# Kernel optimization log

Measured on AMD Instinct MI355X. Metric: run time of the kernel, lower is better.

## Reference

```python
import jax, jax.numpy as jnp
import numpy as np

B, S, H = 32, 4096, 512
N = 2 * H  # n = hidden_size * 2


def setup_inputs() -> dict:
    key = jax.random.key(0)
    ks = jax.random.split(key, 10)
    scale = 1.0 / np.sqrt(N)
    return {
        "dec_in_state": jax.random.normal(ks[0], (B, N), jnp.float32),
        "enc_states": jax.random.normal(ks[1], (B, S, N), jnp.float32),
        "enc_lens": jax.random.randint(ks[2], (B,), 1, S + 1),
        "coverage_vector": jax.random.uniform(ks[3], (B, S), jnp.float32),
        "Wh": jax.random.normal(ks[4], (N, N), jnp.float32) * scale,
        "bh": jnp.zeros((N,), jnp.float32),
        "Ws": jax.random.normal(ks[5], (N, N), jnp.float32) * scale,
        "bs": jnp.zeros((N,), jnp.float32),
        "wc": jax.random.normal(ks[6], (N,), jnp.float32) * scale,  # W_c: Linear(1, N, bias=False)
        "v": jax.random.normal(ks[7], (N,), jnp.float32) * scale,   # v: Linear(N, 1, bias=False)
    }


def reference(dec_in_state, enc_states, enc_lens, coverage_vector, Wh, bh, Ws, bs, wc, v):
    seq_len = enc_states.shape[1]
    # additive Bahdanau features: [B,S,N]
    enc_feats = jnp.einsum("bsn,mn->bsm", enc_states, Wh) + bh
    dec_feats = dec_in_state @ Ws.T + bs  # [B,N]
    cov_feats = coverage_vector[..., None] * wc  # [B,S,N] (Linear(1,N,no bias))
    e = jnp.tanh(enc_feats + dec_feats[:, None, :] + cov_feats) @ v  # [B,S]
    # masked renormalized softmax
    mask = (jnp.arange(seq_len)[None, :] < enc_lens[:, None]).astype(e.dtype)  # [B,S]
    attn = jax.nn.softmax(e, axis=1) * mask
    attn = attn / attn.sum(axis=1, keepdims=True)
    context = jnp.einsum("bs,bsn->bn", attn, enc_states)  # [B,N]
    coverage_out = coverage_vector + attn
    return (context, attn, coverage_out)
```

## Files before the change

kernel.cpp:

```cpp
#include <hip/hip_runtime.h>
#include <math.h>

#define B 32
#define S 4096
#define N 1024

typedef short short8 __attribute__((ext_vector_type(8)));
typedef short short4v __attribute__((ext_vector_type(4)));
typedef float float4v __attribute__((ext_vector_type(4)));

__device__ inline short f2bf(float f) {
    unsigned u = __builtin_bit_cast(unsigned, f);
    u += 0x7fffu + ((u >> 16) & 1u);
    return (short)(u >> 16);
}

__device__ __forceinline__ void load_lds16(const void* g, void* l) {
    __builtin_amdgcn_global_load_lds(
        (const __attribute__((address_space(1))) void*)g,
        (__attribute__((address_space(3))) void*)l, 16, 0, 0);
}

__global__ __launch_bounds__(256)
void prep_cvt_kernel(const float* __restrict__ dec, const float* __restrict__ Ws,
                     const float* __restrict__ bs, const float* __restrict__ enc,
                     const float* __restrict__ Wh, float* __restrict__ dec_feats,
                     float* __restrict__ e, short* __restrict__ encb,
                     short* __restrict__ whb) {
    unsigned bid = blockIdx.x;
    int tid = threadIdx.x;
    if (bid < 2048u) {
        if (bid < 512u) e[bid * 256 + tid] = 0.f;
        const size_t n8e = (size_t)B * S * N / 8;
        for (size_t i = (size_t)bid * 256 + tid; i < n8e; i += 2048u * 256u) {
            const float4v* s = (const float4v*)(enc + i * 8);
            float4v a = s[0], b = s[1];
            short8 o = { f2bf(a.x), f2bf(a.y), f2bf(a.z), f2bf(a.w),
                         f2bf(b.x), f2bf(b.y), f2bf(b.z), f2bf(b.w) };
            *(short8*)(encb + i * 8) = o;
        }
    } else if (bid < 2064u) {
        const size_t n8w = (size_t)N * N / 8;
        for (size_t i = (size_t)(bid - 2048u) * 256 + tid; i < n8w; i += 16u * 256u) {
            const float4v* s = (const float4v*)(Wh + i * 8);
            float4v a = s[0], b = s[1];
            short8 o = { f2bf(a.x), f2bf(a.y), f2bf(a.z), f2bf(a.w),
                         f2bf(b.x), f2bf(b.y), f2bf(b.z), f2bf(b.w) };
            *(short8*)(whb + i * 8) = o;
        }
    } else {
        int wid  = (int)(bid - 2064u) * 4 + (tid >> 6);
        int lane = tid & 63;
        int m = wid >> 5, b = wid & 31;
        const float4* drow = (const float4*)(dec + (size_t)b * N);
        const float4* wrow = (const float4*)(Ws + (size_t)m * N);
        float acc = 0.f;
#pragma unroll
        for (int k = 0; k < 4; ++k) {
            float4 a = drow[lane + (k << 6)];
            float4 w = wrow[lane + (k << 6)];
            acc += a.x * w.x + a.y * w.y + a.z * w.z + a.w * w.w;
        }
        acc += __shfl_xor(acc, 1);  acc += __shfl_xor(acc, 2);
        acc += __shfl_xor(acc, 4);  acc += __shfl_xor(acc, 8);
        acc += __shfl_xor(acc, 16); acc += __shfl_xor(acc, 32);
        if (lane == 0) dec_feats[(size_t)b * N + m] = acc + bs[m];
    }
}

__global__ __launch_bounds__(256)
void prep_kernel(const float* __restrict__ dec, const float* __restrict__ Ws,
                 const float* __restrict__ bs, float* __restrict__ dec_feats,
                 float* __restrict__ e) {
    int tg = blockIdx.x * 256 + threadIdx.x;
    if (tg < B * S) e[tg] = 0.f;
    int wid  = (blockIdx.x << 2) + (threadIdx.x >> 6);
    int lane = threadIdx.x & 63;
    int m = wid >> 5, b = wid & 31;
    const float4* drow = (const float4*)(dec + (size_t)b * N);
    const float4* wrow = (const float4*)(Ws + (size_t)m * N);
    float acc = 0.f;
#pragma unroll
    for (int k = 0; k < 4; ++k) {
        float4 a = drow[lane + (k << 6)];
        float4 w = wrow[lane + (k << 6)];
        acc += a.x * w.x + a.y * w.y + a.z * w.z + a.w * w.w;
    }
    acc += __shfl_xor(acc, 1);  acc += __shfl_xor(acc, 2);
    acc += __shfl_xor(acc, 4);  acc += __shfl_xor(acc, 8);
    acc += __shfl_xor(acc, 16); acc += __shfl_xor(acc, 32);
    if (lane == 0) dec_feats[(size_t)b * N + m] = acc + bs[m];
}

#define REGION_A(slot, hk) ((slot)*16384 + (hk)*8192)
#define REGION_B(slot, hk) (32768 + (slot)*16384 + (hk)*8192)

__global__ __launch_bounds__(512, 2)
void score_mfma8_kernel(const short* __restrict__ encb, const short* __restrict__ whb,
                        const float* __restrict__ bh, const float* __restrict__ dec_feats,
                        const float* __restrict__ cov, const float* __restrict__ wc,
                        const float* __restrict__ v, float* __restrict__ e) {
    __shared__ short lds[65536];

    unsigned bid = blockIdx.x;
    unsigned c = (bid & 7u) * 128u + (bid >> 3);
    int rtp = (int)(c >> 2), mtile = (int)(c & 3u);
    int m0 = mtile * 256;

    int t = threadIdx.x, lane = t & 63, w = t >> 6;
    int wm_ = w >> 2, wn_ = w & 3;
    int cq = lane >> 4, cm = lane & 15;

    int srow = lane >> 2;
    int sg = (lane & 3) ^ ((lane >> 3) & 3);
    const short* bS0 = whb + (size_t)(m0 + w * 16 + srow) * N + sg * 8;
    const short* bS1 = bS0 + (size_t)128 * N;
    const int dc0 = w * 512, dc1 = dc0 + 4096;

    int aoff[8], boff[4];
#pragma unroll
    for (int f = 0; f < 8; ++f) {
        int R = wm_ * 128 + f * 16 + cm;
        aoff[f] = R * 32 + ((cq ^ ((R >> 1) & 3)) << 3);
    }
#pragma unroll
    for (int j = 0; j < 4; ++j) {
        int R = wn_ * 64 + j * 16 + cm;
        boff[j] = R * 32 + ((cq ^ ((R >> 1) & 3)) << 3);
    }

    float basej[4], wcj[4], vj[4];
    {
        int bidx0 = (rtp * 2 * 256) >> 12;
        const float* df = dec_feats + ((size_t)bidx0 << 10);
#pragma unroll
        for (int j = 0; j < 4; ++j) {
            int m = m0 + wn_ * 64 + j * 16 + cm;
            basej[j] = bh[m] + df[m];
            wcj[j]   = wc[m];
            vj[j]    = v[m];
        }
    }

#define STAGE(srcp0, srcp1, region, colElem) do {                         \
        int _cc = (colElem) & (N - 1);                                    \
        load_lds16((srcp0) + _cc, &lds[(region) + dc0]);                  \
        load_lds16((srcp1) + _cc, &lds[(region) + dc1]);                  \
    } while (0)

#define PHASE(slot, sub, SRC0, SRC1, SREGION, SCOL) do {                      \
        const int hk_ = (sub) >> 1, mh_ = (sub) & 1;                          \
        if (mh_ == 0) {                                                       \
            _Pragma("unroll")                                                 \
            for (int j = 0; j < 4; ++j)                                       \
                bf[j] = *(const short8*)&lds[REGION_B(slot, hk_) + boff[j]];  \
        }                                                                     \
        short8 af[4];                                                         \
        _Pragma("unroll")                                                     \
        for (int f = 0; f < 4; ++f)                                           \
            af[f] = *(const short8*)&lds[REGION_A(slot, hk_) + aoff[mh_ * 4 + f]]; \
        STAGE(SRC0, SRC1, SREGION, SCOL);                                     \
        __builtin_amdgcn_s_barrier();                                         \
        asm volatile("s_waitcnt lgkmcnt(0)" ::: "memory");                    \
        __builtin_amdgcn_sched_barrier(0);                                    \
        __builtin_amdgcn_s_setprio(1);                                        \
        _Pragma("unroll")                                                     \
        for (int f = 0; f < 4; ++f)                                           \
            _Pragma("unroll")                                                 \
            for (int j = 0; j < 4; ++j)                                       \
                acc[mh_ * 4 + f][j] = __builtin_amdgcn_mfma_f32_16x16x32_bf16(\
                    af[f], bf[j], acc[mh_ * 4 + f][j], 0, 0, 0);              \
        __builtin_amdgcn_s_setprio(0);                                        \
        if (mh_ == 1) asm volatile("s_waitcnt vmcnt(8)" ::: "memory");        \
        __builtin_amdgcn_s_barrier();                                         \
    } while (0)

#pragma unroll 1
    for (int it = 0; it < 2; ++it) {
        int r0 = (rtp * 2 + it) * 256;
        const short* aS0 = encb + (size_t)(r0 + w * 16 + srow) * N + sg * 8;
        const short* aS1 = aS0 + (size_t)128 * N;

        float4v acc[8][4];
#pragma unroll
        for (int f = 0; f < 8; ++f)
#pragma unroll
            for (int j = 0; j < 4; ++j) acc[f][j] = (float4v){0.f, 0.f, 0.f, 0.f};

        STAGE(aS0, aS1, REGION_A(0, 0), 0);
        STAGE(bS0, bS1, REGION_B(0, 0), 0);
        STAGE(aS0, aS1, REGION_A(0, 1), 32);
        STAGE(bS0, bS1, REGION_B(0, 1), 32);
        STAGE(aS0, aS1, REGION_A(1, 0), 64);
        STAGE(bS0, bS1, REGION_B(1, 0), 64);
        asm volatile("s_waitcnt vmcnt(8)" ::: "memory");
        __builtin_amdgcn_s_barrier();

        short8 bf[4];

#pragma unroll 1
        for (int i = 0; i < 8; ++i) {
            int kb = i * 128;
            PHASE(0, 0, aS0, aS1, REGION_A(1, 1), kb + 96);
            PHASE(0, 1, bS0, bS1, REGION_B(1, 1), kb + 96);
            PHASE(0, 2, aS0, aS1, REGION_A(0, 0), kb + 128);
            PHASE(0, 3, bS0, bS1, REGION_B(0, 0), kb + 128);
            PHASE(1, 0, aS0, aS1, REGION_A(0, 1), kb + 160);
            PHASE(1, 1, bS0, bS1, REGION_B(0, 1), kb + 160);
            PHASE(1, 2, aS0, aS1, REGION_A(1, 0), kb + 192);
            PHASE(1, 3, bS0, bS1, REGION_B(1, 0), kb + 192);
        }
        asm volatile("s_waitcnt vmcnt(0)" ::: "memory");

#pragma unroll
        for (int f = 0; f < 8; ++f) {
            int rbase = r0 + wm_ * 128 + f * 16 + cq * 4;
            float4v cvv = *(const float4v*)&cov[rbase];
            float cv[4] = {cvv.x, cvv.y, cvv.z, cvv.w};
            float rs[4] = {0.f, 0.f, 0.f, 0.f};
#pragma unroll
            for (int j = 0; j < 4; ++j) {
#pragma unroll
                for (int reg = 0; reg < 4; ++reg) {
                    float val = acc[f][j][reg] + basej[j] + cv[reg] * wcj[j];
                    val = fminf(fmaxf(val, -15.f), 15.f);
                    float t2 = __builtin_amdgcn_exp2f(val * 2.8853900817779268f);
                    float r  = __builtin_amdgcn_rcpf(t2 + 1.f);
                    float th = fmaf(-2.f, r, 1.f);
                    rs[reg] = fmaf(th, vj[j], rs[reg]);
                }
            }
#pragma unroll
            for (int reg = 0; reg < 4; ++reg) {
                float p = rs[reg];
                p += __shfl_xor(p, 1);
                p += __shfl_xor(p, 2);
                p += __shfl_xor(p, 4);
                p += __shfl_xor(p, 8);
                if (cm == 0) atomicAdd(&e[rbase + reg], p);
            }
        }
        asm volatile("s_waitcnt vmcnt(0)" ::: "memory");
        __builtin_amdgcn_s_barrier();
    }
#undef PHASE
#undef STAGE
}

#define BR 128
#define BM 128
#define BK 64
#define LDK (BK + 8)

__global__ __launch_bounds__(256)
void score_mfma_kernel(const float* __restrict__ enc, const float* __restrict__ Wh,
                       const float* __restrict__ bh, const float* __restrict__ dec_feats,
                       const float* __restrict__ cov, const float* __restrict__ wc,
                       const float* __restrict__ v, float* __restrict__ e) {
    __shared__ short As[BR][LDK];
    __shared__ short Bs[BM][LDK];

    unsigned h   = blockIdx.x;
    unsigned xcd = h & 7u;
    unsigned mt  = (h >> 3) & 7u;
    unsigned g   = h >> 6;
    int r0 = (int)(xcd + 8u * g) * BR;
    int m0 = (int)mt * BM;

    int t    = threadIdx.x;
    int lane = t & 63;
    int w    = t >> 6;
    int wr   = (w >> 1) * 64;
    int wm   = (w & 1) * 64;
    int cq   = lane >> 4;
    int cm   = lane & 15;

    float4v acc[4][4];
#pragma unroll
    for (int i = 0; i < 4; ++i)
#pragma unroll
        for (int j = 0; j < 4; ++j) acc[i][j] = (float4v){0.f, 0.f, 0.f, 0.f};

    int srow = t >> 4;
    int scol = (t & 15) * 4;

    for (int k0 = 0; k0 < N; k0 += BK) {
#pragma unroll
        for (int p = 0; p < 8; ++p) {
            int row = p * 16 + srow;
            float4v a = *(const float4v*)(enc + (size_t)(r0 + row) * N + k0 + scol);
            short4v ap = { f2bf(a.x), f2bf(a.y), f2bf(a.z), f2bf(a.w) };
            *(short4v*)&As[row][scol] = ap;
            float4v bq = *(const float4v*)(Wh + (size_t)(m0 + row) * N + k0 + scol);
            short4v bp = { f2bf(bq.x), f2bf(bq.y), f2bf(bq.z), f2bf(bq.w) };
            *(short4v*)&Bs[row][scol] = bp;
        }
        __syncthreads();
#pragma unroll
        for (int ks = 0; ks < BK; ks += 32) {
            short8 af[4], bfr[4];
#pragma unroll
            for (int i = 0; i < 4; ++i)
                af[i] = *(const short8*)&As[wr + i * 16 + cm][ks + cq * 8];
#pragma unroll
            for (int j = 0; j < 4; ++j)
                bfr[j] = *(const short8*)&Bs[wm + j * 16 + cm][ks + cq * 8];
#pragma unroll
            for (int i = 0; i < 4; ++i)
#pragma unroll
                for (int j = 0; j < 4; ++j)
                    acc[i][j] = __builtin_amdgcn_mfma_f32_16x16x32_bf16(
                        af[i], bfr[j], acc[i][j], 0, 0, 0);
        }
        __syncthreads();
    }

    int b = r0 >> 12;
    const float* df = dec_feats + ((size_t)b << 10);

    float basej[4], wcj[4], vj[4];
#pragma unroll
    for (int j = 0; j < 4; ++j) {
        int m = m0 + wm + j * 16 + cm;
        basej[j] = bh[m] + df[m];
        wcj[j]   = wc[m];
        vj[j]    = v[m];
    }

#pragma unroll
    for (int i = 0; i < 4; ++i) {
        int rbase = r0 + wr + i * 16 + cq * 4;
        float cv[4];
#pragma unroll
        for (int reg = 0; reg < 4; ++reg) cv[reg] = cov[rbase + reg];
        float rs[4] = {0.f, 0.f, 0.f, 0.f};
#pragma unroll
        for (int j = 0; j < 4; ++j) {
#pragma unroll
            for (int reg = 0; reg < 4; ++reg) {
                float val = acc[i][j][reg] + basej[j] + cv[reg] * wcj[j];
                val = fminf(fmaxf(val, -15.f), 15.f);
                float t2 = __builtin_amdgcn_exp2f(val * 2.8853900817779268f);
                float r  = __builtin_amdgcn_rcpf(t2 + 1.f);
                float th = fmaf(-2.f, r, 1.f);
                rs[reg] = fmaf(th, vj[j], rs[reg]);
            }
        }
#pragma unroll
        for (int reg = 0; reg < 4; ++reg) {
            float p = rs[reg];
            p += __shfl_xor(p, 1);
            p += __shfl_xor(p, 2);
            p += __shfl_xor(p, 4);
            p += __shfl_xor(p, 8);
            if (cm == 0) atomicAdd(&e[rbase + reg], p);
        }
    }
}

__global__ __launch_bounds__(1024)
void softmax_kernel(const float* __restrict__ e, const int* __restrict__ lens,
                    const float* __restrict__ cov,
                    float* __restrict__ attn, float* __restrict__ cov_out) {
    int b = blockIdx.x, t = threadIdx.x;
    int lane = t & 63, wid = t >> 6;
    int len = lens[b];
    const float* eb = e + (size_t)b * S;
    __shared__ float redm[16], reds[16];

    float ev[4];
    float mx = -INFINITY;
#pragma unroll
    for (int k = 0; k < 4; ++k) {
        int s = t + (k << 10);
        ev[k] = (s < len) ? eb[s] : -INFINITY;
        mx = fmaxf(mx, ev[k]);
    }
    mx = fmaxf(mx, __shfl_xor(mx, 1));  mx = fmaxf(mx, __shfl_xor(mx, 2));
    mx = fmaxf(mx, __shfl_xor(mx, 4));  mx = fmaxf(mx, __shfl_xor(mx, 8));
    mx = fmaxf(mx, __shfl_xor(mx, 16)); mx = fmaxf(mx, __shfl_xor(mx, 32));
    if (lane == 0) redm[wid] = mx;
    __syncthreads();
    if (t < 16) {
        float v2 = redm[t];
        v2 = fmaxf(v2, __shfl_xor(v2, 1)); v2 = fmaxf(v2, __shfl_xor(v2, 2));
        v2 = fmaxf(v2, __shfl_xor(v2, 4)); v2 = fmaxf(v2, __shfl_xor(v2, 8));
        if (t == 0) redm[0] = v2;
    }
    __syncthreads();
    mx = redm[0];

    float ex[4];
    float sum = 0.f;
#pragma unroll
    for (int k = 0; k < 4; ++k) {
        ex[k] = exp2f((ev[k] - mx) * 1.4426950408889634f);
        sum += ex[k];
    }
    sum += __shfl_xor(sum, 1);  sum += __shfl_xor(sum, 2);
    sum += __shfl_xor(sum, 4);  sum += __shfl_xor(sum, 8);
    sum += __shfl_xor(sum, 16); sum += __shfl_xor(sum, 32);
    if (lane == 0) reds[wid] = sum;
    __syncthreads();
    if (t < 16) {
        float v2 = reds[t];
        v2 += __shfl_xor(v2, 1); v2 += __shfl_xor(v2, 2);
        v2 += __shfl_xor(v2, 4); v2 += __shfl_xor(v2, 8);
        if (t == 0) reds[0] = v2;
    }
    __syncthreads();
    float inv = 1.f / reds[0];

#pragma unroll
    for (int k = 0; k < 4; ++k) {
        int s = t + (k << 10);
        float a = ex[k] * inv;
        attn[(size_t)b * S + s] = a;
        cov_out[(size_t)b * S + s] = cov[(size_t)b * S + s] + a;
    }
}

#define SCH 64
__global__ __launch_bounds__(256)
void context_part_kernel(const float* __restrict__ attn, const float* __restrict__ enc,
                         float* __restrict__ part) {
    int b  = blockIdx.y;
    int ch = blockIdx.x;
    int s0 = ch * (S / SCH);
    int n4 = threadIdx.x;
    const float4* ep = (const float4*)(enc + ((size_t)b * S + s0) * N);
    float4 acc = {0.f, 0.f, 0.f, 0.f};
    for (int s = 0; s < S / SCH; ++s) {
        float a = attn[(size_t)b * S + s0 + s];
        float4 ev = ep[(size_t)s * (N / 4) + n4];
        acc.x += a * ev.x; acc.y += a * ev.y;
        acc.z += a * ev.z; acc.w += a * ev.w;
    }
    *(float4*)&part[((size_t)b * SCH + ch) * N + n4 * 4] = acc;
}

__global__ __launch_bounds__(256)
void context_reduce_kernel(const float* __restrict__ part, float* __restrict__ ctx) {
    int idx = blockIdx.x * 256 + threadIdx.x;
    int b = idx >> 10, n = idx & (N - 1);
    const float* p = part + (size_t)b * SCH * N + n;
    float acc = 0.f;
#pragma unroll
    for (int c2 = 0; c2 < SCH; ++c2) acc += p[(size_t)c2 * N];
    ctx[idx] = acc;
}

__global__ __launch_bounds__(256)
void context_kernel(const float* __restrict__ attn, const float* __restrict__ enc,
                    float* __restrict__ ctx) {
    int b  = blockIdx.y;
    int s0 = blockIdx.x * (S / SCH);
    int n4 = threadIdx.x;
    const float4* ep = (const float4*)(enc + ((size_t)b * S + s0) * N);
    float4 acc = {0.f, 0.f, 0.f, 0.f};
    for (int s = 0; s < S / SCH; ++s) {
        float a = attn[(size_t)b * S + s0 + s];
        float4 ev = ep[(size_t)s * (N / 4) + n4];
        acc.x += a * ev.x; acc.y += a * ev.y;
        acc.z += a * ev.z; acc.w += a * ev.w;
    }
    float* cp = ctx + (size_t)b * N + n4 * 4;
    atomicAdd(cp + 0, acc.x);
    atomicAdd(cp + 1, acc.y);
    atomicAdd(cp + 2, acc.z);
    atomicAdd(cp + 3, acc.w);
}

extern "C" void kernel_launch(void* const* d_in, const int* in_sizes, int n_in,
                              void* d_out, int out_size, void* d_ws, size_t ws_size,
                              hipStream_t stream) {
    const float* dec  = (const float*)d_in[0];
    const float* enc  = (const float*)d_in[1];
    const int*   lens = (const int*)  d_in[2];
    const float* cov  = (const float*)d_in[3];
    const float* Wh   = (const float*)d_in[4];
    const float* bh   = (const float*)d_in[5];
    const float* Ws   = (const float*)d_in[6];
    const float* bs   = (const float*)d_in[7];
    const float* wc   = (const float*)d_in[8];
    const float* v    = (const float*)d_in[9];

    float* out     = (float*)d_out;
    float* ctx     = out;
    float* attn    = out + (size_t)B * N;
    float* cov_out = attn + (size_t)B * S;

    size_t off_e    = (size_t)B * N * 4;
    size_t off_encb = off_e + (size_t)B * S * 4;
    size_t off_whb  = off_encb + (size_t)B * S * N * 2;
    size_t off_part = off_whb + (size_t)N * N * 2;
    size_t need     = off_part + (size_t)B * SCH * N * 4;

    float* dec_feats = (float*)d_ws;
    float* e         = (float*)((char*)d_ws + off_e);

    if (ws_size >= need) {
        short* encb = (short*)((char*)d_ws + off_encb);
        short* whb  = (short*)((char*)d_ws + off_whb);
        float* part = (float*)((char*)d_ws + off_part);
        prep_cvt_kernel<<<10256, 256, 0, stream>>>(dec, Ws, bs, enc, Wh,
                                                   dec_feats, e, encb, whb);
        score_mfma8_kernel<<<1024, 512, 0, stream>>>(
            encb, whb, bh, dec_feats, cov, wc, v, e);
        softmax_kernel<<<B, 1024, 0, stream>>>(e, lens, cov, attn, cov_out);
        context_part_kernel<<<dim3(SCH, B), 256, 0, stream>>>(attn, enc, part);
        context_reduce_kernel<<<(B * N) / 256, 256, 0, stream>>>(part, ctx);
    } else {
        prep_kernel<<<8192, 256, 0, stream>>>(dec, Ws, bs, dec_feats, e);
        hipMemsetAsync(ctx, 0, (size_t)B * N * sizeof(float), stream);
        score_mfma_kernel<<<(B * S / BR) * (N / BM), 256, 0, stream>>>(
            enc, Wh, bh, dec_feats, cov, wc, v, e);
        softmax_kernel<<<B, 1024, 0, stream>>>(e, lens, cov, attn, cov_out);
        context_kernel<<<dim3(SCH, B), 256, 0, stream>>>(attn, enc, ctx);
    }
}
```

Measured before the change: 1.156 ms.

## Split softmax into chunked partials and fuse normalization into context kernel

Replaces the 32-block softmax kernel with a per-chunk partial max/sum kernel over 8x32 blocks, then has the context kernel combine the partials, compute attn and coverage_out, and use the weights from LDS directly. The aim is to remove a low-parallelism softmax launch and a global round-trip of attn. The score GEMM grid is also halved to 512 blocks, each processing four row tiles instead of two, which amortizes per-block setup but reduces parallelism. Each context block recomputes the global max and sum from 8 partials, which is redundant but small.

```diff
diff --git a/kernel.cpp b/kernel.cpp
--- a/kernel.cpp
+++ b/kernel.cpp
@@ -4,6 +4,7 @@
 #define B 32
 #define S 4096
 #define N 1024
+#define L2E 1.4426950408889634f
 
 typedef short short8 __attribute__((ext_vector_type(8)));
 typedef short short4v __attribute__((ext_vector_type(4)));
@@ -103,8 +104,8 @@
     __shared__ short lds[65536];
 
     unsigned bid = blockIdx.x;
-    unsigned c = (bid & 7u) * 128u + (bid >> 3);
-    int rtp = (int)(c >> 2), mtile = (int)(c & 3u);
+    unsigned c = (bid & 7u) * 64u + (bid >> 3);
+    int rtq = (int)(c >> 2), mtile = (int)(c & 3u);
     int m0 = mtile * 256;
 
     int t = threadIdx.x, lane = t & 63, w = t >> 6;
@@ -131,7 +132,7 @@
 
     float basej[4], wcj[4], vj[4];
     {
-        int bidx0 = (rtp * 2 * 256) >> 12;
+        int bidx0 = rtq >> 2;
         const float* df = dec_feats + ((size_t)bidx0 << 10);
 #pragma unroll
         for (int j = 0; j < 4; ++j) {
@@ -176,8 +177,8 @@
     } while (0)
 
 #pragma unroll 1
-    for (int it = 0; it < 2; ++it) {
-        int r0 = (rtp * 2 + it) * 256;
+    for (int it = 0; it < 4; ++it) {
+        int r0 = (rtq * 4 + it) * 256;
         const short* aS0 = encb + (size_t)(r0 + w * 16 + srow) * N + sg * 8;
         const short* aS1 = aS0 + (size_t)128 * N;
 
@@ -358,6 +359,93 @@
     }
 }
 
+__global__ __launch_bounds__(256)
+void softmax_partial_kernel(const float* __restrict__ e, const int* __restrict__ lens,
+                            float2* __restrict__ pm) {
+    int b = blockIdx.y, ch = blockIdx.x;
+    int t = threadIdx.x, lane = t & 63, wid = t >> 6;
+    int len = lens[b];
+    int s0 = ch * 512;
+    const float* eb = e + (size_t)b * S + s0;
+    float v0 = (s0 + t       < len) ? eb[t]       : -INFINITY;
+    float v1 = (s0 + t + 256 < len) ? eb[t + 256] : -INFINITY;
+    float mx = fmaxf(v0, v1);
+    mx = fmaxf(mx, __shfl_xor(mx, 1));  mx = fmaxf(mx, __shfl_xor(mx, 2));
+    mx = fmaxf(mx, __shfl_xor(mx, 4));  mx = fmaxf(mx, __shfl_xor(mx, 8));
+    mx = fmaxf(mx, __shfl_xor(mx, 16)); mx = fmaxf(mx, __shfl_xor(mx, 32));
+    __shared__ float redm[4], reds[4];
+    if (lane == 0) redm[wid] = mx;
+    __syncthreads();
+    mx = fmaxf(fmaxf(redm[0], redm[1]), fmaxf(redm[2], redm[3]));
+
+    float sum = 0.f;
+    if (mx > -INFINITY)
+        sum = exp2f((v0 - mx) * L2E) + exp2f((v1 - mx) * L2E);
+    sum += __shfl_xor(sum, 1);  sum += __shfl_xor(sum, 2);
+    sum += __shfl_xor(sum, 4);  sum += __shfl_xor(sum, 8);
+    sum += __shfl_xor(sum, 16); sum += __shfl_xor(sum, 32);
+    if (lane == 0) reds[wid] = sum;
+    __syncthreads();
+    if (t == 0) {
+        float2 p; p.x = mx; p.y = reds[0] + reds[1] + reds[2] + reds[3];
+        pm[b * 8 + ch] = p;
+    }
+}
+
+#define SCH 64
+__global__ __launch_bounds__(256)
+void context_part_kernel(const float* __restrict__ e, const int* __restrict__ lens,
+                         const float2* __restrict__ pm, const float* __restrict__ cov,
+                         const float* __restrict__ enc, float* __restrict__ attn,
+                         float* __restrict__ cov_out, float* __restrict__ part) {
+    int b  = blockIdx.y;
+    int ch = blockIdx.x;
+    int s0 = ch * (S / SCH);
+    int tid = threadIdx.x;
+    __shared__ float a_lds[S / SCH];
+
+    if (tid < S / SCH) {
+        int len = lens[b];
+        const float2* pb = pm + b * 8;
+        float M = -INFINITY;
+#pragma unroll
+        for (int i = 0; i < 8; ++i) M = fmaxf(M, pb[i].x);
+        float Ssum = 0.f;
+#pragma unroll
+        for (int i = 0; i < 8; ++i)
+            Ssum += pb[i].y * exp2f((pb[i].x - M) * L2E);
+        float inv = 1.f / Ssum;
+        int s = s0 + tid;
+        float ew = e[(size_t)b * S + s];
+        float a = (s < len) ? exp2f((ew - M) * L2E) * inv : 0.f;
+        a_lds[tid] = a;
+        attn[(size_t)b * S + s] = a;
+        cov_out[(size_t)b * S + s] = cov[(size_t)b * S + s] + a;
+    }
+    __syncthreads();
+
+    const float4* ep = (const float4*)(enc + ((size_t)b * S + s0) * N);
+    float4 acc = {0.f, 0.f, 0.f, 0.f};
+    for (int s = 0; s < S / SCH; ++s) {
+        float a = a_lds[s];
+        float4 ev = ep[(size_t)s * (N / 4) + tid];
+        acc.x += a * ev.x; acc.y += a * ev.y;
+        acc.z += a * ev.z; acc.w += a * ev.w;
+    }
+    *(float4*)&part[((size_t)b * SCH + ch) * N + tid * 4] = acc;
+}
+
+__global__ __launch_bounds__(256)
+void context_reduce_kernel(const float* __restrict__ part, float* __restrict__ ctx) {
+    int idx = blockIdx.x * 256 + threadIdx.x;
+    int b = idx >> 10, n = idx & (N - 1);
+    const float* p = part + (size_t)b * SCH * N + n;
+    float acc = 0.f;
+#pragma unroll
+    for (int c2 = 0; c2 < SCH; ++c2) acc += p[(size_t)c2 * N];
+    ctx[idx] = acc;
+}
+
 __global__ __launch_bounds__(1024)
 void softmax_kernel(const float* __restrict__ e, const int* __restrict__ lens,
                     const float* __restrict__ cov,
@@ -394,7 +482,8 @@
     float sum = 0.f;
 #pragma unroll
     for (int k = 0; k < 4; ++k) {
-        ex[k] = exp2f((ev[k] - mx) * 1.4426950408889634f);
+        int s = t + (k << 10);
+        ex[k] = exp2f((ev[k] - mx) * L2E);
         sum += ex[k];
     }
     sum += __shfl_xor(sum, 1);  sum += __shfl_xor(sum, 2);
@@ -418,36 +507,6 @@
         attn[(size_t)b * S + s] = a;
         cov_out[(size_t)b * S + s] = cov[(size_t)b * S + s] + a;
     }
-}
-
-#define SCH 64
-__global__ __launch_bounds__(256)
-void context_part_kernel(const float* __restrict__ attn, const float* __restrict__ enc,
-                         float* __restrict__ part) {
-    int b  = blockIdx.y;
-    int ch = blockIdx.x;
-    int s0 = ch * (S / SCH);
-    int n4 = threadIdx.x;
-    const float4* ep = (const float4*)(enc + ((size_t)b * S + s0) * N);
-    float4 acc = {0.f, 0.f, 0.f, 0.f};
-    for (int s = 0; s < S / SCH; ++s) {
-        float a = attn[(size_t)b * S + s0 + s];
-        float4 ev = ep[(size_t)s * (N / 4) + n4];
-        acc.x += a * ev.x; acc.y += a * ev.y;
-        acc.z += a * ev.z; acc.w += a * ev.w;
-    }
-    *(float4*)&part[((size_t)b * SCH + ch) * N + n4 * 4] = acc;
-}
-
-__global__ __launch_bounds__(256)
-void context_reduce_kernel(const float* __restrict__ part, float* __restrict__ ctx) {
-    int idx = blockIdx.x * 256 + threadIdx.x;
-    int b = idx >> 10, n = idx & (N - 1);
-    const float* p = part + (size_t)b * SCH * N + n;
-    float acc = 0.f;
-#pragma unroll
-    for (int c2 = 0; c2 < SCH; ++c2) acc += p[(size_t)c2 * N];
-    ctx[idx] = acc;
 }
 
 __global__ __launch_bounds__(256)
@@ -494,21 +553,24 @@
     size_t off_encb = off_e + (size_t)B * S * 4;
     size_t off_whb  = off_encb + (size_t)B * S * N * 2;
     size_t off_part = off_whb + (size_t)N * N * 2;
-    size_t need     = off_part + (size_t)B * SCH * N * 4;
+    size_t off_pm   = off_part + (size_t)B * SCH * N * 4;
+    size_t need     = off_pm + (size_t)B * 8 * sizeof(float2);
 
     float* dec_feats = (float*)d_ws;
     float* e         = (float*)((char*)d_ws + off_e);
 
     if (ws_size >= need) {
-        short* encb = (short*)((char*)d_ws + off_encb);
-        short* whb  = (short*)((char*)d_ws + off_whb);
-        float* part = (float*)((char*)d_ws + off_part);
+        short*  encb = (short*)((char*)d_ws + off_encb);
+        short*  whb  = (short*)((char*)d_ws + off_whb);
+        float*  part = (float*)((char*)d_ws + off_part);
+        float2* pm   = (float2*)((char*)d_ws + off_pm);
         prep_cvt_kernel<<<10256, 256, 0, stream>>>(dec, Ws, bs, enc, Wh,
                                                    dec_feats, e, encb, whb);
-        score_mfma8_kernel<<<1024, 512, 0, stream>>>(
+        score_mfma8_kernel<<<512, 512, 0, stream>>>(
             encb, whb, bh, dec_feats, cov, wc, v, e);
-        softmax_kernel<<<B, 1024, 0, stream>>>(e, lens, cov, attn, cov_out);
-        context_part_kernel<<<dim3(SCH, B), 256, 0, stream>>>(attn, enc, part);
+        softmax_partial_kernel<<<dim3(8, B), 256, 0, stream>>>(e, lens, pm);
+        context_part_kernel<<<dim3(SCH, B), 256, 0, stream>>>(
+            e, lens, pm, cov, enc, attn, cov_out, part);
         context_reduce_kernel<<<(B * N) / 256, 256, 0, stream>>>(part, ctx);
     } else {
         prep_kernel<<<8192, 256, 0, stream>>>(dec, Ws, bs, dec_feats, e);
```

Result: no change. 1.165 ms (+0.7%).
